# Kernel tuning notes

Measured on AMD Instinct MI355X. Metric: run time of the kernel, lower is better.

The kernel has to match this reference:

```python
import jax, jax.numpy as jnp
import numpy as np

D_HEAD = 64  # module's self.heads scaling constant


def setup_inputs() -> dict:
    key = jax.random.key(0)
    kq, kk, kv = jax.random.split(key, 3)
    N, HW, C = 4, 4096, 64
    Q = jax.random.normal(kq, (N, HW, C), dtype=jnp.float32)
    K = jax.random.normal(kk, (N, HW, C), dtype=jnp.float32)
    V = jax.random.normal(kv, (N, HW, C), dtype=jnp.float32)
    return {"Q": Q, "K": K, "V": V}


def reference(Q, K, V):
    # logits[n, q, k] = Q[n,q,:] . K[n,k,:] / sqrt(d_head)
    scale = 1.0 / jnp.sqrt(jnp.asarray(D_HEAD, dtype=Q.dtype))
    logits = jnp.einsum("nqc,nkc->nqk", Q, K) * scale  # [N, HW, HW]
    # NOTE: softmax over the QUERY axis (dim=1), non-standard
    attn = jax.nn.softmax(logits, axis=1)
    return jnp.einsum("nqk,nkc->nqc", attn, V)
```

## Files before the change

kernel.cpp:

```cpp
#include <hip/hip_runtime.h>

#define NB 4
#define HWN 4096
#define CD 64
#define NSTRIDE (HWN * CD)

typedef short short8 __attribute__((ext_vector_type(8), may_alias));
typedef float f32x4 __attribute__((ext_vector_type(4), may_alias));

__device__ constexpr float C1 = 0.18033688011112042f;

__device__ __forceinline__ unsigned short f2bf(float f) {
    unsigned u = __builtin_bit_cast(unsigned, f);
    u = (u + 0x7FFFu + ((u >> 16) & 1u)) >> 16;
    return (unsigned short)u;
}

__device__ __forceinline__ float fexp2(float x) {
#if __has_builtin(__builtin_amdgcn_exp2f)
    return __builtin_amdgcn_exp2f(x);
#else
    return exp2f(x);
#endif
}

__device__ __forceinline__ size_t qk_swz(int row, int c) {
    return (size_t)(row >> 4) * 1024 + (c >> 5) * 512 +
           ((((c >> 3) & 3) * 16 + (row & 15)) * 8) + (c & 7);
}

__global__ __launch_bounds__(256) void cvt_qk(const float* __restrict__ Q,
                                              const float* __restrict__ K,
                                              unsigned short* __restrict__ Qs,
                                              unsigned short* __restrict__ Ks) {
    int i = (blockIdx.x * 256 + threadIdx.x) * 4;
    int rg = i >> 6, c = i & 63;
    int n = rg >> 12, r = rg & 4095;
    float4 q = *(const float4*)(Q + i);
    float4 k = *(const float4*)(K + i);
    ushort4 qo, ko;
    qo.x = f2bf(q.x * C1); qo.y = f2bf(q.y * C1);
    qo.z = f2bf(q.z * C1); qo.w = f2bf(q.w * C1);
    ko.x = f2bf(k.x); ko.y = f2bf(k.y); ko.z = f2bf(k.z); ko.w = f2bf(k.w);
    size_t off = (size_t)n * NSTRIDE + qk_swz(r, c);
    *(ushort4*)(Qs + off) = qo;
    *(ushort4*)(Ks + off) = ko;
}

__global__ __attribute__((amdgpu_flat_work_group_size(256, 256), amdgpu_waves_per_eu(4, 8)))
void lsum_kernel(const unsigned short* __restrict__ Qs,
                 const unsigned short* __restrict__ Ks,
                 float* __restrict__ l) {
    int tid = threadIdx.x;
    int w = tid >> 6, lane = tid & 63, quad = lane >> 4, m16 = lane & 15;
    int n = blockIdx.y;
    int kbase = blockIdx.x * 128 + w * 32;

    const unsigned short* Kp = Ks + (size_t)n * NSTRIDE + (kbase >> 4) * 1024 + lane * 8;
    short8 ka0 = *(const short8*)(Kp);
    short8 ka1 = *(const short8*)(Kp + 512);
    short8 kb0 = *(const short8*)(Kp + 1024);
    short8 kb1 = *(const short8*)(Kp + 1536);

    const unsigned short* Qp = Qs + (size_t)n * NSTRIDE + blockIdx.z * 16384 + lane * 8;

    short8 qc0 = *(const short8*)(Qp);
    short8 qc1 = *(const short8*)(Qp + 512);
    Qp += 1024;

    float lA[4] = {0.f, 0.f, 0.f, 0.f};
    float lB[4] = {0.f, 0.f, 0.f, 0.f};
#pragma unroll 2
    for (int qc = 0; qc < 16; ++qc) {
        short8 qn0 = *(const short8*)(Qp);
        short8 qn1 = *(const short8*)(Qp + 512);
        f32x4 a = {0.f, 0.f, 0.f, 0.f}, b = {0.f, 0.f, 0.f, 0.f};
        a = __builtin_amdgcn_mfma_f32_16x16x32_bf16(ka0, qc0, a, 0, 0, 0);
        a = __builtin_amdgcn_mfma_f32_16x16x32_bf16(ka1, qc1, a, 0, 0, 0);
        b = __builtin_amdgcn_mfma_f32_16x16x32_bf16(kb0, qc0, b, 0, 0, 0);
        b = __builtin_amdgcn_mfma_f32_16x16x32_bf16(kb1, qc1, b, 0, 0, 0);
#pragma unroll
        for (int r = 0; r < 4; ++r) {
            lA[r] += fexp2(a[r]);
            lB[r] += fexp2(b[r]);
        }
        qc0 = qn0; qc1 = qn1;
        Qp += 1024;
    }
#pragma unroll
    for (int r = 0; r < 4; ++r)
        for (int d = 1; d < 16; d <<= 1) {
            lA[r] += __shfl_xor(lA[r], d);
            lB[r] += __shfl_xor(lB[r], d);
        }
    if (m16 == 0) {
        float* lp = l + n * HWN + kbase + quad * 4;
#pragma unroll
        for (int r = 0; r < 4; ++r) {
            atomicAdd(lp + r, lA[r]);
            atomicAdd(lp + 16 + r, lB[r]);
        }
    }
}

__global__ __launch_bounds__(256) void prep_v(const float* __restrict__ V,
                                              const float* __restrict__ l,
                                              unsigned short* __restrict__ Vts) {
    __shared__ float rl[64];
    __shared__ float tile[64][65];
    int tid = threadIdx.x, n = blockIdx.y, kbase = blockIdx.x * 64;
    if (tid < 64) rl[tid] = 1.0f / l[n * HWN + kbase + tid];
    __syncthreads();
#pragma unroll
    for (int i = 0; i < 16; ++i) {
        int e = i * 256 + tid;
        int k = e >> 6, c = e & 63;
        tile[c][k] = V[((size_t)(n * HWN + kbase + k)) * CD + c] * rl[k];
    }
    __syncthreads();
#pragma unroll
    for (int i = 0; i < 2; ++i) {
        int s = i * 256 + tid;
        int c = s >> 3, kg = s & 7;
        int kl = kg * 8;
        int kgl = kbase + kl;
        short8 v;
#pragma unroll
        for (int j = 0; j < 8; ++j) v[j] = (short)f2bf(tile[c][kl + j]);
        size_t off = (size_t)n * NSTRIDE + (size_t)(kgl >> 5) * 2048 + (c >> 4) * 512 +
                     ((((kgl >> 3) & 3) * 16 + (c & 15)) * 8);
        *(short8*)(Vts + off) = v;
    }
}

__global__ __attribute__((amdgpu_flat_work_group_size(256, 256), amdgpu_waves_per_eu(2, 4)))
void attn_kernel(const unsigned short* __restrict__ Qs,
                 const unsigned short* __restrict__ Ks,
                 const unsigned short* __restrict__ Vts,
                 float* __restrict__ partial,
                 int nit) {
    __shared__ short plds[4][2][16][40];
    int tid = threadIdx.x;
    int w = tid >> 6, lane = tid & 63, quad = lane >> 4, m16 = lane & 15;
    int n = blockIdx.y;
    int qbase = blockIdx.x * 64 + w * 16;

    const unsigned short* Qp = Qs + (size_t)n * NSTRIDE + (qbase >> 4) * 1024 + lane * 8;
    short8 qf0 = *(const short8*)(Qp);
    short8 qf1 = *(const short8*)(Qp + 512);

    size_t kofs = (size_t)blockIdx.z * (size_t)nit * 2048;
    const unsigned short* Kp = Ks + (size_t)n * NSTRIDE + kofs + lane * 8;
    const unsigned short* Vp = Vts + (size_t)n * NSTRIDE + kofs + lane * 8;

    f32x4 o[4];
#pragma unroll
    for (int ct = 0; ct < 4; ++ct) o[ct] = f32x4{0.f, 0.f, 0.f, 0.f};

    short* pw0 = &plds[w][0][0][0];
    short* pw1 = &plds[w][1][0][0];
    int wr_off = (quad * 4) * 40 + m16;
    int rd_off = m16 * 40 + quad * 8;

    short8 kc0, kc1, kc2, kc3, vp0, vp1, vp2, vp3;

    kc0 = *(const short8*)(Kp);
    kc1 = *(const short8*)(Kp + 512);
    kc2 = *(const short8*)(Kp + 1024);
    kc3 = *(const short8*)(Kp + 1536);
    Kp += 2048;
    vp0 = *(const short8*)(Vp);
    vp1 = *(const short8*)(Vp + 512);
    vp2 = *(const short8*)(Vp + 1024);
    vp3 = *(const short8*)(Vp + 1536);
    Vp += 2048;
    {
        f32x4 s0 = {0.f, 0.f, 0.f, 0.f}, s1 = {0.f, 0.f, 0.f, 0.f};
        s0 = __builtin_amdgcn_mfma_f32_16x16x32_bf16(qf0, kc0, s0, 0, 0, 0);
        s0 = __builtin_amdgcn_mfma_f32_16x16x32_bf16(qf1, kc1, s0, 0, 0, 0);
        s1 = __builtin_amdgcn_mfma_f32_16x16x32_bf16(qf0, kc2, s1, 0, 0, 0);
        s1 = __builtin_amdgcn_mfma_f32_16x16x32_bf16(qf1, kc3, s1, 0, 0, 0);
        short* prow = pw0 + wr_off;
#pragma unroll
        for (int rr = 0; rr < 4; ++rr) {
            prow[rr * 40]      = (short)f2bf(fexp2(s0[rr]));
            prow[rr * 40 + 16] = (short)f2bf(fexp2(s1[rr]));
        }
    }
    kc0 = *(const short8*)(Kp);
    kc1 = *(const short8*)(Kp + 512);
    kc2 = *(const short8*)(Kp + 1024);
    kc3 = *(const short8*)(Kp + 1536);
    Kp += 2048;

#pragma unroll 2
    for (int it = 1; it < nit; ++it) {
        short8 kn0 = *(const short8*)(Kp);
        short8 kn1 = *(const short8*)(Kp + 512);
        short8 kn2 = *(const short8*)(Kp + 1024);
        short8 kn3 = *(const short8*)(Kp + 1536);
        Kp += 2048;
        short8 vn0 = *(const short8*)(Vp);
        short8 vn1 = *(const short8*)(Vp + 512);
        short8 vn2 = *(const short8*)(Vp + 1024);
        short8 vn3 = *(const short8*)(Vp + 1536);
        Vp += 2048;

        f32x4 s0 = {0.f, 0.f, 0.f, 0.f}, s1 = {0.f, 0.f, 0.f, 0.f};
        s0 = __builtin_amdgcn_mfma_f32_16x16x32_bf16(qf0, kc0, s0, 0, 0, 0);
        s0 = __builtin_amdgcn_mfma_f32_16x16x32_bf16(qf1, kc1, s0, 0, 0, 0);
        s1 = __builtin_amdgcn_mfma_f32_16x16x32_bf16(qf0, kc2, s1, 0, 0, 0);
        s1 = __builtin_amdgcn_mfma_f32_16x16x32_bf16(qf1, kc3, s1, 0, 0, 0);

        short* pr = ((it & 1) ? pw0 : pw1) + rd_off;
        short8 pf = *(const short8*)pr;
#pragma unroll
        for (int ct = 0; ct < 4; ++ct) {
            short8 vf;
            switch (ct) { case 0: vf = vp0; break; case 1: vf = vp1; break;
                          case 2: vf = vp2; break; default: vf = vp3; }
            o[ct] = __builtin_amdgcn_mfma_f32_16x16x32_bf16(pf, vf, o[ct], 0, 0, 0);
        }

        short* prow = ((it & 1) ? pw1 : pw0) + wr_off;
#pragma unroll
        for (int rr = 0; rr < 4; ++rr) {
            prow[rr * 40]      = (short)f2bf(fexp2(s0[rr]));
            prow[rr * 40 + 16] = (short)f2bf(fexp2(s1[rr]));
        }

        kc0 = kn0; kc1 = kn1; kc2 = kn2; kc3 = kn3;
        vp0 = vn0; vp1 = vn1; vp2 = vn2; vp3 = vn3;
    }

    {
        short* pr = ((nit & 1) ? pw0 : pw1) + rd_off;
        short8 pf = *(const short8*)pr;
        o[0] = __builtin_amdgcn_mfma_f32_16x16x32_bf16(pf, vp0, o[0], 0, 0, 0);
        o[1] = __builtin_amdgcn_mfma_f32_16x16x32_bf16(pf, vp1, o[1], 0, 0, 0);
        o[2] = __builtin_amdgcn_mfma_f32_16x16x32_bf16(pf, vp2, o[2], 0, 0, 0);
        o[3] = __builtin_amdgcn_mfma_f32_16x16x32_bf16(pf, vp3, o[3], 0, 0, 0);
    }

    float* pp = partial + (size_t)blockIdx.z * (NB * HWN * CD) +
                ((size_t)(n * HWN + qbase + quad * 4)) * CD + m16;
#pragma unroll
    for (int ct = 0; ct < 4; ++ct)
#pragma unroll
        for (int rr = 0; rr < 4; ++rr)
            pp[rr * CD + ct * 16] = o[ct][rr];
}

__global__ __launch_bounds__(256) void reduce_out(const float* __restrict__ p,
                                                  float* __restrict__ out, int ns) {
    int i = (blockIdx.x * 256 + threadIdx.x) * 4;
    f32x4 a = *(const f32x4*)(p + i);
    for (int s = 1; s < ns; ++s)
        a = a + *(const f32x4*)(p + (size_t)s * (NB * HWN * CD) + i);
    *(f32x4*)(out + i) = a;
}

extern "C" void kernel_launch(void* const* d_in, const int* in_sizes, int n_in,
                              void* d_out, int out_size, void* d_ws, size_t ws_size,
                              hipStream_t stream) {
    const float* Q = (const float*)d_in[0];
    const float* K = (const float*)d_in[1];
    const float* V = (const float*)d_in[2];
    float* out = (float*)d_out;

    char* ws = (char*)d_ws;
    unsigned short* Qs  = (unsigned short*)(ws);
    unsigned short* Ks  = (unsigned short*)(ws + (1u << 21));
    unsigned short* Vts = (unsigned short*)(ws + (2u << 21));
    float* l       = (float*)(ws + (3u << 21));
    float* partial = (float*)(ws + (4u << 21));

    size_t base = (size_t)(4u << 21);
    size_t slice = (size_t)NB * HWN * CD * sizeof(float);
    int ns = (ws_size >= base + 4 * slice) ? 4 : 2;
    int nit = HWN / ns / 32;

    (void)hipMemsetAsync(l, 0, (size_t)NB * HWN * sizeof(float), stream);

    cvt_qk<<<1024, 256, 0, stream>>>(Q, K, Qs, Ks);
    lsum_kernel<<<dim3(32, NB, 16), 256, 0, stream>>>(Qs, Ks, l);
    prep_v<<<dim3(64, NB), 256, 0, stream>>>(V, l, Vts);
    attn_kernel<<<dim3(64, NB, ns), 256, 0, stream>>>(Qs, Ks, Vts, partial, nit);
    reduce_out<<<1024, 256, 0, stream>>>(partial, out, ns);
}
```

Measured before the change: 119.6 us.

## Double per-wave tile work in lsum and attn kernels, raise key split

```diff
diff --git a/kernel.cpp b/kernel.cpp
--- a/kernel.cpp
+++ b/kernel.cpp
@@ -47,20 +47,24 @@
     *(ushort4*)(Ks + off) = ko;
 }
 
-__global__ __attribute__((amdgpu_flat_work_group_size(256, 256), amdgpu_waves_per_eu(4, 8)))
+__global__ __attribute__((amdgpu_flat_work_group_size(256, 256), amdgpu_waves_per_eu(2, 4)))
 void lsum_kernel(const unsigned short* __restrict__ Qs,
                  const unsigned short* __restrict__ Ks,
                  float* __restrict__ l) {
     int tid = threadIdx.x;
     int w = tid >> 6, lane = tid & 63, quad = lane >> 4, m16 = lane & 15;
     int n = blockIdx.y;
-    int kbase = blockIdx.x * 128 + w * 32;
+    int kbase = blockIdx.x * 256 + w * 64;
 
     const unsigned short* Kp = Ks + (size_t)n * NSTRIDE + (kbase >> 4) * 1024 + lane * 8;
     short8 ka0 = *(const short8*)(Kp);
     short8 ka1 = *(const short8*)(Kp + 512);
     short8 kb0 = *(const short8*)(Kp + 1024);
     short8 kb1 = *(const short8*)(Kp + 1536);
+    short8 kc0 = *(const short8*)(Kp + 2048);
+    short8 kc1 = *(const short8*)(Kp + 2560);
+    short8 kd0 = *(const short8*)(Kp + 3072);
+    short8 kd1 = *(const short8*)(Kp + 3584);
 
     const unsigned short* Qp = Qs + (size_t)n * NSTRIDE + blockIdx.z * 16384 + lane * 8;
 
@@ -70,28 +74,38 @@
 
     float lA[4] = {0.f, 0.f, 0.f, 0.f};
     float lB[4] = {0.f, 0.f, 0.f, 0.f};
+    float lC[4] = {0.f, 0.f, 0.f, 0.f};
+    float lD[4] = {0.f, 0.f, 0.f, 0.f};
 #pragma unroll 2
     for (int qc = 0; qc < 16; ++qc) {
         short8 qn0 = *(const short8*)(Qp);
         short8 qn1 = *(const short8*)(Qp + 512);
-        f32x4 a = {0.f, 0.f, 0.f, 0.f}, b = {0.f, 0.f, 0.f, 0.f};
+        f32x4 a = {0.f, 0.f, 0.f, 0.f}, b = a, c = a, d = a;
         a = __builtin_amdgcn_mfma_f32_16x16x32_bf16(ka0, qc0, a, 0, 0, 0);
         a = __builtin_amdgcn_mfma_f32_16x16x32_bf16(ka1, qc1, a, 0, 0, 0);
         b = __builtin_amdgcn_mfma_f32_16x16x32_bf16(kb0, qc0, b, 0, 0, 0);
         b = __builtin_amdgcn_mfma_f32_16x16x32_bf16(kb1, qc1, b, 0, 0, 0);
+        c = __builtin_amdgcn_mfma_f32_16x16x32_bf16(kc0, qc0, c, 0, 0, 0);
+        c = __builtin_amdgcn_mfma_f32_16x16x32_bf16(kc1, qc1, c, 0, 0, 0);
+        d = __builtin_amdgcn_mfma_f32_16x16x32_bf16(kd0, qc0, d, 0, 0, 0);
+        d = __builtin_amdgcn_mfma_f32_16x16x32_bf16(kd1, qc1, d, 0, 0, 0);
 #pragma unroll
         for (int r = 0; r < 4; ++r) {
             lA[r] += fexp2(a[r]);
             lB[r] += fexp2(b[r]);
+            lC[r] += fexp2(c[r]);
+            lD[r] += fexp2(d[r]);
         }
         qc0 = qn0; qc1 = qn1;
         Qp += 1024;
     }
 #pragma unroll
     for (int r = 0; r < 4; ++r)
-        for (int d = 1; d < 16; d <<= 1) {
-            lA[r] += __shfl_xor(lA[r], d);
-            lB[r] += __shfl_xor(lB[r], d);
+        for (int d1 = 1; d1 < 16; d1 <<= 1) {
+            lA[r] += __shfl_xor(lA[r], d1);
+            lB[r] += __shfl_xor(lB[r], d1);
+            lC[r] += __shfl_xor(lC[r], d1);
+            lD[r] += __shfl_xor(lD[r], d1);
         }
     if (m16 == 0) {
         float* lp = l + n * HWN + kbase + quad * 4;
@@ -99,6 +113,8 @@
         for (int r = 0; r < 4; ++r) {
             atomicAdd(lp + r, lA[r]);
             atomicAdd(lp + 16 + r, lB[r]);
+            atomicAdd(lp + 32 + r, lC[r]);
+            atomicAdd(lp + 48 + r, lD[r]);
         }
     }
 }
@@ -139,26 +155,26 @@
                  const unsigned short* __restrict__ Vts,
                  float* __restrict__ partial,
                  int nit) {
-    __shared__ short plds[4][2][16][40];
+    __shared__ short plds[4][2][2][16][40];
     int tid = threadIdx.x;
     int w = tid >> 6, lane = tid & 63, quad = lane >> 4, m16 = lane & 15;
     int n = blockIdx.y;
-    int qbase = blockIdx.x * 64 + w * 16;
+    int qbase = blockIdx.x * 128 + w * 16;
 
     const unsigned short* Qp = Qs + (size_t)n * NSTRIDE + (qbase >> 4) * 1024 + lane * 8;
     short8 qf0 = *(const short8*)(Qp);
     short8 qf1 = *(const short8*)(Qp + 512);
+    short8 qg0 = *(const short8*)(Qp + 4096);
+    short8 qg1 = *(const short8*)(Qp + 4096 + 512);
 
     size_t kofs = (size_t)blockIdx.z * (size_t)nit * 2048;
     const unsigned short* Kp = Ks + (size_t)n * NSTRIDE + kofs + lane * 8;
     const unsigned short* Vp = Vts + (size_t)n * NSTRIDE + kofs + lane * 8;
 
-    f32x4 o[4];
-#pragma unroll
-    for (int ct = 0; ct < 4; ++ct) o[ct] = f32x4{0.f, 0.f, 0.f, 0.f};
-
-    short* pw0 = &plds[w][0][0][0];
-    short* pw1 = &plds[w][1][0][0];
+    f32x4 oA[4], oB[4];
+#pragma unroll
+    for (int ct = 0; ct < 4; ++ct) { oA[ct] = f32x4{0.f, 0.f, 0.f, 0.f}; oB[ct] = oA[ct]; }
+
     int wr_off = (quad * 4) * 40 + m16;
     int rd_off = m16 * 40 + quad * 8;
 
@@ -175,16 +191,23 @@
     vp3 = *(const short8*)(Vp + 1536);
     Vp += 2048;
     {
-        f32x4 s0 = {0.f, 0.f, 0.f, 0.f}, s1 = {0.f, 0.f, 0.f, 0.f};
-        s0 = __builtin_amdgcn_mfma_f32_16x16x32_bf16(qf0, kc0, s0, 0, 0, 0);
-        s0 = __builtin_amdgcn_mfma_f32_16x16x32_bf16(qf1, kc1, s0, 0, 0, 0);
-        s1 = __builtin_amdgcn_mfma_f32_16x16x32_bf16(qf0, kc2, s1, 0, 0, 0);
-        s1 = __builtin_amdgcn_mfma_f32_16x16x32_bf16(qf1, kc3, s1, 0, 0, 0);
-        short* prow = pw0 + wr_off;
+        f32x4 sA0 = {0.f, 0.f, 0.f, 0.f}, sA1 = sA0, sB0 = sA0, sB1 = sA0;
+        sA0 = __builtin_amdgcn_mfma_f32_16x16x32_bf16(qf0, kc0, sA0, 0, 0, 0);
+        sA0 = __builtin_amdgcn_mfma_f32_16x16x32_bf16(qf1, kc1, sA0, 0, 0, 0);
+        sA1 = __builtin_amdgcn_mfma_f32_16x16x32_bf16(qf0, kc2, sA1, 0, 0, 0);
+        sA1 = __builtin_amdgcn_mfma_f32_16x16x32_bf16(qf1, kc3, sA1, 0, 0, 0);
+        sB0 = __builtin_amdgcn_mfma_f32_16x16x32_bf16(qg0, kc0, sB0, 0, 0, 0);
+        sB0 = __builtin_amdgcn_mfma_f32_16x16x32_bf16(qg1, kc1, sB0, 0, 0, 0);
+        sB1 = __builtin_amdgcn_mfma_f32_16x16x32_bf16(qg0, kc2, sB1, 0, 0, 0);
+        sB1 = __builtin_amdgcn_mfma_f32_16x16x32_bf16(qg1, kc3, sB1, 0, 0, 0);
+        short* pA = &plds[w][0][0][0][0] + wr_off;
+        short* pB = &plds[w][0][1][0][0] + wr_off;
 #pragma unroll
         for (int rr = 0; rr < 4; ++rr) {
-            prow[rr * 40]      = (short)f2bf(fexp2(s0[rr]));
-            prow[rr * 40 + 16] = (short)f2bf(fexp2(s1[rr]));
+            pA[rr * 40]      = (short)f2bf(fexp2(sA0[rr]));
+            pA[rr * 40 + 16] = (short)f2bf(fexp2(sA1[rr]));
+            pB[rr * 40]      = (short)f2bf(fexp2(sB0[rr]));
+            pB[rr * 40 + 16] = (short)f2bf(fexp2(sB1[rr]));
         }
     }
     kc0 = *(const short8*)(Kp);
@@ -193,7 +216,6 @@
     kc3 = *(const short8*)(Kp + 1536);
     Kp += 2048;
 
-#pragma unroll 2
     for (int it = 1; it < nit; ++it) {
         short8 kn0 = *(const short8*)(Kp);
         short8 kn1 = *(const short8*)(Kp + 512);
@@ -206,27 +228,41 @@
         short8 vn3 = *(const short8*)(Vp + 1536);
         Vp += 2048;
 
-        f32x4 s0 = {0.f, 0.f, 0.f, 0.f}, s1 = {0.f, 0.f, 0.f, 0.f};
-        s0 = __builtin_amdgcn_mfma_f32_16x16x32_bf16(qf0, kc0, s0, 0, 0, 0);
-        s0 = __builtin_amdgcn_mfma_f32_16x16x32_bf16(qf1, kc1, s0, 0, 0, 0);
-        s1 = __builtin_amdgcn_mfma_f32_16x16x32_bf16(qf0, kc2, s1, 0, 0, 0);
-        s1 = __builtin_amdgcn_mfma_f32_16x16x32_bf16(qf1, kc3, s1, 0, 0, 0);
-
-        short* pr = ((it & 1) ? pw0 : pw1) + rd_off;
-        short8 pf = *(const short8*)pr;
-#pragma unroll
-        for (int ct = 0; ct < 4; ++ct) {
-            short8 vf;
-            switch (ct) { case 0: vf = vp0; break; case 1: vf = vp1; break;
-                          case 2: vf = vp2; break; default: vf = vp3; }
-            o[ct] = __builtin_amdgcn_mfma_f32_16x16x32_bf16(pf, vf, o[ct], 0, 0, 0);
-        }
-
-        short* prow = ((it & 1) ? pw1 : pw0) + wr_off;
-#pragma unroll
-        for (int rr = 0; rr < 4; ++rr) {
-            prow[rr * 40]      = (short)f2bf(fexp2(s0[rr]));
-            prow[rr * 40 + 16] = (short)f2bf(fexp2(s1[rr]));
+        f32x4 sA0 = {0.f, 0.f, 0.f, 0.f}, sA1 = sA0, sB0 = sA0, sB1 = sA0;
+        sA0 = __builtin_amdgcn_mfma_f32_16x16x32_bf16(qf0, kc0, sA0, 0, 0, 0);
+        sA0 = __builtin_amdgcn_mfma_f32_16x16x32_bf16(qf1, kc1, sA0, 0, 0, 0);
+        sA1 = __builtin_amdgcn_mfma_f32_16x16x32_bf16(qf0, kc2, sA1, 0, 0, 0);
+        sA1 = __builtin_amdgcn_mfma_f32_16x16x32_bf16(qf1, kc3, sA1, 0, 0, 0);
+        sB0 = __builtin_amdgcn_mfma_f32_16x16x32_bf16(qg0, kc0, sB0, 0, 0, 0);
+        sB0 = __builtin_amdgcn_mfma_f32_16x16x32_bf16(qg1, kc1, sB0, 0, 0, 0);
+        sB1 = __builtin_amdgcn_mfma_f32_16x16x32_bf16(qg0, kc2, sB1, 0, 0, 0);
+        sB1 = __builtin_amdgcn_mfma_f32_16x16x32_bf16(qg1, kc3, sB1, 0, 0, 0);
+
+        {
+            int pb = (it - 1) & 1;
+            short8 pfA = *(const short8*)(&plds[w][pb][0][0][0] + rd_off);
+            short8 pfB = *(const short8*)(&plds[w][pb][1][0][0] + rd_off);
+            oA[0] = __builtin_amdgcn_mfma_f32_16x16x32_bf16(pfA, vp0, oA[0], 0, 0, 0);
+            oA[1] = __builtin_amdgcn_mfma_f32_16x16x32_bf16(pfA, vp1, oA[1], 0, 0, 0);
+            oA[2] = __builtin_amdgcn_mfma_f32_16x16x32_bf16(pfA, vp2, oA[2], 0, 0, 0);
+            oA[3] = __builtin_amdgcn_mfma_f32_16x16x32_bf16(pfA, vp3, oA[3], 0, 0, 0);
+            oB[0] = __builtin_amdgcn_mfma_f32_16x16x32_bf16(pfB, vp0, oB[0], 0, 0, 0);
+            oB[1] = __builtin_amdgcn_mfma_f32_16x16x32_bf16(pfB, vp1, oB[1], 0, 0, 0);
+            oB[2] = __builtin_amdgcn_mfma_f32_16x16x32_bf16(pfB, vp2, oB[2], 0, 0, 0);
+            oB[3] = __builtin_amdgcn_mfma_f32_16x16x32_bf16(pfB, vp3, oB[3], 0, 0, 0);
+        }
+
+        {
+            int pb = it & 1;
+            short* pA = &plds[w][pb][0][0][0] + wr_off;
+            short* pB = &plds[w][pb][1][0][0] + wr_off;
+#pragma unroll
+            for (int rr = 0; rr < 4; ++rr) {
+                pA[rr * 40]      = (short)f2bf(fexp2(sA0[rr]));
+                pA[rr * 40 + 16] = (short)f2bf(fexp2(sA1[rr]));
+                pB[rr * 40]      = (short)f2bf(fexp2(sB0[rr]));
+                pB[rr * 40 + 16] = (short)f2bf(fexp2(sB1[rr]));
+            }
         }
 
         kc0 = kn0; kc1 = kn1; kc2 = kn2; kc3 = kn3;
@@ -234,12 +270,17 @@
     }
 
     {
-        short* pr = ((nit & 1) ? pw0 : pw1) + rd_off;
-        short8 pf = *(const short8*)pr;
-        o[0] = __builtin_amdgcn_mfma_f32_16x16x32_bf16(pf, vp0, o[0], 0, 0, 0);
-        o[1] = __builtin_amdgcn_mfma_f32_16x16x32_bf16(pf, vp1, o[1], 0, 0, 0);
-        o[2] = __builtin_amdgcn_mfma_f32_16x16x32_bf16(pf, vp2, o[2], 0, 0, 0);
-        o[3] = __builtin_amdgcn_mfma_f32_16x16x32_bf16(pf, vp3, o[3], 0, 0, 0);
+        int pb = (nit - 1) & 1;
+        short8 pfA = *(const short8*)(&plds[w][pb][0][0][0] + rd_off);
+        short8 pfB = *(const short8*)(&plds[w][pb][1][0][0] + rd_off);
+        oA[0] = __builtin_amdgcn_mfma_f32_16x16x32_bf16(pfA, vp0, oA[0], 0, 0, 0);
+        oA[1] = __builtin_amdgcn_mfma_f32_16x16x32_bf16(pfA, vp1, oA[1], 0, 0, 0);
+        oA[2] = __builtin_amdgcn_mfma_f32_16x16x32_bf16(pfA, vp2, oA[2], 0, 0, 0);
+        oA[3] = __builtin_amdgcn_mfma_f32_16x16x32_bf16(pfA, vp3, oA[3], 0, 0, 0);
+        oB[0] = __builtin_amdgcn_mfma_f32_16x16x32_bf16(pfB, vp0, oB[0], 0, 0, 0);
+        oB[1] = __builtin_amdgcn_mfma_f32_16x16x32_bf16(pfB, vp1, oB[1], 0, 0, 0);
+        oB[2] = __builtin_amdgcn_mfma_f32_16x16x32_bf16(pfB, vp2, oB[2], 0, 0, 0);
+        oB[3] = __builtin_amdgcn_mfma_f32_16x16x32_bf16(pfB, vp3, oB[3], 0, 0, 0);
     }
 
     float* pp = partial + (size_t)blockIdx.z * (NB * HWN * CD) +
@@ -247,8 +288,10 @@
 #pragma unroll
     for (int ct = 0; ct < 4; ++ct)
 #pragma unroll
-        for (int rr = 0; rr < 4; ++rr)
-            pp[rr * CD + ct * 16] = o[ct][rr];
+        for (int rr = 0; rr < 4; ++rr) {
+            pp[rr * CD + ct * 16] = oA[ct][rr];
+            pp[(64 + rr) * CD + ct * 16] = oB[ct][rr];
+        }
 }
 
 __global__ __launch_bounds__(256) void reduce_out(const float* __restrict__ p,
@@ -277,14 +320,15 @@
 
     size_t base = (size_t)(4u << 21);
     size_t slice = (size_t)NB * HWN * CD * sizeof(float);
-    int ns = (ws_size >= base + 4 * slice) ? 4 : 2;
+    int ns = (ws_size >= base + 8 * slice) ? 8
+           : (ws_size >= base + 4 * slice) ? 4 : 2;
     int nit = HWN / ns / 32;
 
     (void)hipMemsetAsync(l, 0, (size_t)NB * HWN * sizeof(float), stream);
 
     cvt_qk<<<1024, 256, 0, stream>>>(Q, K, Qs, Ks);
-    lsum_kernel<<<dim3(32, NB, 16), 256, 0, stream>>>(Qs, Ks, l);
+    lsum_kernel<<<dim3(16, NB, 16), 256, 0, stream>>>(Qs, Ks, l);
     prep_v<<<dim3(64, NB), 256, 0, stream>>>(V, l, Vts);
-    attn_kernel<<<dim3(64, NB, ns), 256, 0, stream>>>(Qs, Ks, Vts, partial, nit);
+    attn_kernel<<<dim3(32, NB, ns), 256, 0, stream>>>(Qs, Ks, Vts, partial, nit);
     reduce_out<<<1024, 256, 0, stream>>>(partial, out, ns);
 }
```

After: 115.0 us. 1.04x faster.
